# Optimization experiments

Hardware: AMD Instinct MI355X
Metric: run time of the kernel (lower is better)

Reference implementation:

```python
import jax, jax.numpy as jnp
import numpy as np

D = 1024
H = 16
HD = D // H
FF = 4096
EPS = 1e-5
B, L = 8, 1024

def setup_inputs() -> dict:
    key = jax.random.key(0)
    ks = jax.random.split(key, 12)
    s = lambda k, shape: jax.random.normal(k, shape, dtype=jnp.float32) * (shape[0] ** -0.5)
    return {
        "x": jax.random.normal(ks[0], (B, L, D), dtype=jnp.float32),
        "attention_mask": jnp.ones((B, L), dtype=jnp.int32),
        "wq": s(ks[1], (D, D)), "bq": jnp.zeros((D,), jnp.float32),
        "wk": s(ks[2], (D, D)), "bk": jnp.zeros((D,), jnp.float32),
        "wv": s(ks[3], (D, D)), "bv": jnp.zeros((D,), jnp.float32),
        "wo": s(ks[4], (D, D)), "bo": jnp.zeros((D,), jnp.float32),
        "ln1_s": jnp.ones((D,), jnp.float32), "ln1_b": jnp.zeros((D,), jnp.float32),
        "ln2_s": jnp.ones((D,), jnp.float32), "ln2_b": jnp.zeros((D,), jnp.float32),
        "w1": s(ks[5], (D, FF)), "b1": jnp.zeros((FF,), jnp.float32),
        "w2": s(ks[6], (FF, D)), "b2": jnp.zeros((D,), jnp.float32),
    }

def _layer_norm(x, scale, bias):
    mu = jnp.mean(x, axis=-1, keepdims=True)
    var = jnp.mean(jnp.square(x - mu), axis=-1, keepdims=True)
    return (x - mu) * jax.lax.rsqrt(var + EPS) * scale + bias

def _quick_gelu(x):
    return x * jax.nn.sigmoid(1.702 * x)

def reference(x, attention_mask, wq, bq, wk, bk, wv, bv, wo, bo,
              ln1_s, ln1_b, ln2_s, ln2_b, w1, b1, w2, b2):
    Bc, Lc, Dc = x.shape
    scale = HD ** -0.5
    # --- attention block (pre-LN) ---
    h = _layer_norm(x, ln1_s, ln1_b)
    to_heads = lambda t: t.reshape(Bc, Lc, H, HD).transpose(0, 2, 1, 3)
    q = to_heads(h @ wq + bq)
    k = to_heads(h @ wk + bk)
    v = to_heads(h @ wv + bv)
    scores = jnp.einsum('bhqd,bhkd->bhqk', q.astype(jnp.float32), k.astype(jnp.float32)) * scale
    fmask = jnp.where(attention_mask[:, None, None, :] > 0, 0.0,
                      jnp.finfo(scores.dtype).min)
    weights = jax.nn.softmax(scores + fmask, axis=-1)
    attn = jnp.einsum('bhqk,bhkd->bhqd', weights, v.astype(jnp.float32))
    attn = attn.transpose(0, 2, 1, 3).reshape(Bc, Lc, Dc).astype(x.dtype)
    x = x + (attn @ wo + bo)
    # --- MLP block (pre-LN) ---
    h = _layer_norm(x, ln2_s, ln2_b)
    h = _quick_gelu(h @ w1 + b1) @ w2 + b2
    return x + h
```

## Files before the change

### kernel.cpp

```cpp
#include <hip/hip_runtime.h>
#include <math.h>

#define D_MODEL 1024
#define N_TOK   8192
#define SEQ_L   1024
#define N_HEAD  16
#define HEAD_D  64
#define FF_DIM  4096

typedef __attribute__((ext_vector_type(8))) short bf16x8;
typedef __attribute__((ext_vector_type(4))) short short4v;
typedef __attribute__((ext_vector_type(2))) int  int2v;
typedef __attribute__((ext_vector_type(4))) float f32x4;

#define MFMA16(a, b, c) __builtin_amdgcn_mfma_f32_16x16x32_bf16((a), (b), (c), 0, 0, 0)

#define GLD16(gp, lp) __builtin_amdgcn_global_load_lds(                      \
    (const __attribute__((address_space(1))) void*)(gp),                     \
    (__attribute__((address_space(3))) void*)(lp), 16, 0, 0)

#if defined(__has_builtin)
#if __has_builtin(__builtin_amdgcn_exp2f)
#define EXP2F(x) __builtin_amdgcn_exp2f(x)
#else
#define EXP2F(x) exp2f(x)
#endif
#else
#define EXP2F(x) exp2f(x)
#endif

__device__ __forceinline__ short f2bf(float f) {
    unsigned u = __float_as_uint(f);
    u += 0x7fffu + ((u >> 16) & 1u);
    return (short)(u >> 16);
}

__device__ __forceinline__ int pack2bf(float a, float b) {
    unsigned ua = __float_as_uint(a) + 0x8000u;
    unsigned ub = __float_as_uint(b) + 0x8000u;
    return __builtin_amdgcn_perm(ub, ua, 0x07060302u);
}

__device__ __forceinline__ unsigned ldsoff(const void* p) {
    return (unsigned)(size_t)(const __attribute__((address_space(3))) void*)p;
}

__device__ __forceinline__ bf16x8 dsr(unsigned off) {
    bf16x8 d;
    asm volatile("ds_read_b128 %0, %1" : "=v"(d) : "v"(off));
    return d;
}

__global__ __launch_bounds__(256) void ln_kernel(const float* __restrict__ x,
                                                 const float* __restrict__ g,
                                                 const float* __restrict__ b,
                                                 short* __restrict__ o)
{
    int t = blockIdx.x;
    const float* xr = x + (size_t)t * D_MODEL;
    short* orow = o + (size_t)t * D_MODEL;
    float vals[4];
    float lsum = 0.f, lsq = 0.f;
#pragma unroll
    for (int i = 0; i < 4; i++) {
        float v = xr[threadIdx.x + i * 256];
        vals[i] = v; lsum += v; lsq += v * v;
    }
#pragma unroll
    for (int off = 32; off > 0; off >>= 1) {
        lsum += __shfl_down(lsum, off);
        lsq  += __shfl_down(lsq,  off);
    }
    __shared__ float red[8];
    int wid = threadIdx.x >> 6, lane = threadIdx.x & 63;
    if (lane == 0) { red[wid] = lsum; red[4 + wid] = lsq; }
    __syncthreads();
    if (threadIdx.x == 0) {
        red[0] = red[0] + red[1] + red[2] + red[3];
        red[4] = red[4] + red[5] + red[6] + red[7];
    }
    __syncthreads();
    float mean = red[0] * (1.f / D_MODEL);
    float var  = red[4] * (1.f / D_MODEL) - mean * mean;
    float inv  = rsqrtf(var + 1e-5f);
#pragma unroll
    for (int i = 0; i < 4; i++) {
        int c = threadIdx.x + i * 256;
        orow[c] = f2bf((vals[i] - mean) * inv * g[c] + b[c]);
    }
}

__global__ __launch_bounds__(256) void prep_kernel(
    const float* __restrict__ wq, const float* __restrict__ wk,
    const float* __restrict__ wv, const float* __restrict__ wo,
    const float* __restrict__ w1, const float* __restrict__ w2,
    const int*   __restrict__ amask,
    short* __restrict__ wqkvt, short* __restrict__ wot,
    short* __restrict__ w1t,  short* __restrict__ w2t,
    float* __restrict__ fmask)
{
    int id = blockIdx.x;
    if (id >= 12288) {
        int i = (id - 12288) * 256 + threadIdx.x;
        fmask[i] = (amask[i] > 0) ? 0.f : -1e30f;
        return;
    }
    const float* src; short* dst; int R, C, tloc, csh;
    if (id < 4096) {
        int wsel = id >> 10; tloc = id & 1023; R = 1024; C = 1024; csh = 5;
        src = (wsel == 0) ? wq : (wsel == 1) ? wk : (wsel == 2) ? wv : wo;
        dst = (wsel == 3) ? wot : (wqkvt + (size_t)wsel * 1024 * 1024);
    } else if (id < 8192) {
        tloc = id - 4096; R = 1024; C = 4096; csh = 7; src = w1; dst = w1t;
    } else {
        tloc = id - 8192; R = 4096; C = 1024; csh = 5; src = w2; dst = w2t;
    }
    int ty = tloc >> csh, tx = tloc & ((1 << csh) - 1);
    int r0 = ty * 32, c0 = tx * 32;
    __shared__ float t[32][33];
    int tid = threadIdx.x;
#pragma unroll
    for (int i = 0; i < 4; i++) {
        int idx = i * 256 + tid;
        int r = idx >> 5, c = idx & 31;
        t[r][c] = src[(size_t)(r0 + r) * C + c0 + c];
    }
    __syncthreads();
#pragma unroll
    for (int i = 0; i < 4; i++) {
        int idx = i * 256 + tid;
        int rr = idx >> 5, cc = idx & 31;
        dst[(size_t)(c0 + rr) * R + r0 + cc] = f2bf(t[cc][rr]);
    }
}

template<int DBUF>
__global__ __launch_bounds__(256) void gemm_bf16(
    const short* __restrict__ A, int lda,
    const short* __restrict__ Bt, int ldb,
    const float* __restrict__ bias,
    const float* __restrict__ bias2,
    const float* __restrict__ bias3,
    const float* __restrict__ resid,
    float* __restrict__ Cf, short* __restrict__ Cb, short* __restrict__ Cvt,
    int ldc, int K, int act, int qkv, int gx)
{
    __shared__ __align__(16) short sA[(1 + DBUF) * 8192];
    __shared__ __align__(16) short sB[(1 + DBUF) * 8192];
    const int tid = threadIdx.x;
    const int lane = tid & 63, wave = tid >> 6;
    const int quad = lane >> 4, l15 = lane & 15;

    const int id = blockIdx.x;
    const int xcd = id & 7, j = id >> 3;
    const int bx = j % gx, by = xcd + 8 * (j / gx);
    const int bm = by * 128, bn = bx * 128;
    const int wm = (wave >> 1) * 64, wn = (wave & 1) * 64;

    const int lr = lane >> 3;
    const int lc = (lane & 7) ^ lr;
    const int sw = l15 & 7;

    const short* Ab = A  + (size_t)(bm + wave * 32 + lr) * lda + lc * 8;
    const short* Bb = Bt + (size_t)(bn + wave * 32 + lr) * ldb + lc * 8;

    f32x4 acc[4][4];
#pragma unroll
    for (int i = 0; i < 4; i++)
#pragma unroll
        for (int jj = 0; jj < 4; jj++) acc[i][jj] = (f32x4){0.f, 0.f, 0.f, 0.f};

    const int nk = K >> 6;

    if (DBUF) {
#pragma unroll
        for (int c = 0; c < 4; c++) {
            int cid = wave * 4 + c;
            GLD16(Ab + (size_t)(c * 8) * lda, &sA[cid * 512]);
            GLD16(Bb + (size_t)(c * 8) * ldb, &sB[cid * 512]);
        }
    }

    for (int ki = 0; ki < nk; ki++) {
        __syncthreads();
        if (DBUF) {
            if (ki + 1 < nk) {
                int k0 = (ki + 1) << 6, nb = (ki + 1) & 1;
#pragma unroll
                for (int c = 0; c < 4; c++) {
                    int cid = wave * 4 + c;
                    GLD16(Ab + (size_t)(c * 8) * lda + k0, &sA[nb * 8192 + cid * 512]);
                    GLD16(Bb + (size_t)(c * 8) * ldb + k0, &sB[nb * 8192 + cid * 512]);
                }
            }
        } else {
            int k0 = ki << 6;
#pragma unroll
            for (int c = 0; c < 4; c++) {
                int cid = wave * 4 + c;
                GLD16(Ab + (size_t)(c * 8) * lda + k0, &sA[cid * 512]);
                GLD16(Bb + (size_t)(c * 8) * ldb + k0, &sB[cid * 512]);
            }
            __syncthreads();
        }
        const short* cA = &sA[DBUF ? (ki & 1) * 8192 : 0];
        const short* cB = &sB[DBUF ? (ki & 1) * 8192 : 0];
#pragma unroll
        for (int ko = 0; ko < 2; ko++) {
            bf16x8 af[4], bfr[4];
#pragma unroll
            for (int mt = 0; mt < 4; mt++) {
                int row = wm + mt * 16 + l15;
                af[mt] = *(const bf16x8*)&cA[(row * 8 + ((ko * 4 + quad) ^ sw)) * 8];
            }
#pragma unroll
            for (int nt = 0; nt < 4; nt++) {
                int row = wn + nt * 16 + l15;
                bfr[nt] = *(const bf16x8*)&cB[(row * 8 + ((ko * 4 + quad) ^ sw)) * 8];
            }
#pragma unroll
            for (int mt = 0; mt < 4; mt++)
#pragma unroll
                for (int nt = 0; nt < 4; nt++)
                    acc[mt][nt] = MFMA16(af[mt], bfr[nt], acc[mt][nt]);
        }
    }

#pragma unroll
    for (int mt = 0; mt < 4; mt++)
#pragma unroll
        for (int nt = 0; nt < 4; nt++) {
            int row0 = bm + wm + mt * 16 + quad * 4;
            int col  = bn + wn + nt * 16 + l15;
            if (qkv) {
                int seg = col >> 10, cloc = col & 1023;
                const float* bp = (seg == 0) ? bias : (seg == 1) ? bias2 : bias3;
                float bval = bp[cloc];
                if (seg == 2) {
                    int bb = row0 >> 10, l0 = row0 & 1023;
                    size_t page = (size_t)(bb * N_HEAD + (cloc >> 6)) * HEAD_D + (cloc & 63);
                    short4v pk = { f2bf(acc[mt][nt][0] + bval), f2bf(acc[mt][nt][1] + bval),
                                   f2bf(acc[mt][nt][2] + bval), f2bf(acc[mt][nt][3] + bval) };
                    *(short4v*)&Cvt[page * SEQ_L + l0] = pk;
                } else {
                    short* dst = Cb + (size_t)seg * ((size_t)N_TOK * D_MODEL);
#pragma unroll
                    for (int r = 0; r < 4; r++)
                        dst[(size_t)(row0 + r) * D_MODEL + cloc] = f2bf(acc[mt][nt][r] + bval);
                }
            } else {
#pragma unroll
                for (int r = 0; r < 4; r++) {
                    int row = row0 + r;
                    float v = acc[mt][nt][r] + bias[col];
                    if (act) v = v / (1.f + __expf(-1.702f * v));
                    if (resid) v += resid[(size_t)row * ldc + col];
                    if (Cb) Cb[(size_t)row * ldc + col] = f2bf(v);
                    else    Cf[(size_t)row * ldc + col] = v;
                }
            }
        }
}

#define BAR() __builtin_amdgcn_s_barrier()
#define WAIT_LGKM0() do { asm volatile("s_waitcnt lgkmcnt(0)");               \
                          __builtin_amdgcn_sched_barrier(0); } while (0)

#define STA(buf, h, tt) do {                                                  \
    const short* s_ = Asrc + (size_t)((h) * 128) * lda + (size_t)(tt) * 64;   \
    GLD16(s_,                    &sAs[(buf)*16384 + (h)*8192        + wave*512]); \
    GLD16(s_ + (size_t)64 * lda, &sAs[(buf)*16384 + (h)*8192 + 4096 + wave*512]); \
} while (0)

#define STB(buf, h, tt) do {                                                  \
    if constexpr (NREP == 4) {                                                \
        const short* s_ = Bsrc + (size_t)((h) * 128) * ldb + (size_t)(tt) * 64; \
        GLD16(s_,                    &sBs[(buf)*16384 + (h)*8192        + wave*512]); \
        GLD16(s_ + (size_t)64 * ldb, &sBs[(buf)*16384 + (h)*8192 + 4096 + wave*512]); \
    } else {                                                                  \
        const short* s_ = Bsrc + (size_t)((h) * 64) * ldb + (size_t)(tt) * 64; \
        GLD16(s_, &sBs[(buf)*8192 + (h)*4096 + wave*512]);                    \
    }                                                                         \
} while (0)

#define VMCNT() do {                                                          \
    if constexpr (NREP == 4) asm volatile("s_waitcnt vmcnt(6)");              \
    else                     asm volatile("s_waitcnt vmcnt(4)");              \
} while (0)

#define RDB(buf, nt) do {                                                     \
    unsigned r_ = bBase + (buf) * BUFB + ((unsigned)(wn + (nt)*16 + l15) << 7); \
    bfr[nt][0] = dsr(r_ + c0); bfr[nt][1] = dsr(r_ + c1);                     \
} while (0)
#define RDA(buf, mt8) do {                                                    \
    unsigned r_ = aBase + (buf) * 32768u + ((unsigned)(wm + (mt8)*16 + l15) << 7); \
    afr[(mt8) & 3][0] = dsr(r_ + c0); afr[(mt8) & 3][1] = dsr(r_ + c1);       \
} while (0)

#define PH_MFMA(mh, nh)                                                       \
    __builtin_amdgcn_s_setprio(1);                                            \
    _Pragma("unroll")                                                         \
    for (int mt = 0; mt < 4; mt++)                                            \
        _Pragma("unroll")                                                     \
        for (int nt = 0; nt < NREP / 2; nt++) {                               \
            acc[(mh)*4 + mt][(nh)*(NREP/2) + nt] =                            \
                MFMA16(afr[mt][0], bfr[(nh)*(NREP/2) + nt][0],                \
                       acc[(mh)*4 + mt][(nh)*(NREP/2) + nt]);                 \
            acc[(mh)*4 + mt][(nh)*(NREP/2) + nt] =                            \
                MFMA16(afr[mt][1], bfr[(nh)*(NREP/2) + nt][1],                \
                       acc[(mh)*4 + mt][(nh)*(NREP/2) + nt]);                 \
        }                                                                     \
    __builtin_amdgcn_s_setprio(0);

template<int NREP>
__global__ __launch_bounds__(512, 2) void gemm256(
    const short* __restrict__ A, int lda,
    const short* __restrict__ Bt, int ldb,
    const float* __restrict__ bias,
    const float* __restrict__ bias2,
    const float* __restrict__ bias3,
    const float* __restrict__ resid,
    float* __restrict__ Cf, short* __restrict__ Cb, short* __restrict__ Cvt,
    int ldc, int K, int act, int qkv, int gx)
{
    constexpr int BN = NREP * 64;
    constexpr unsigned BUFB = (unsigned)BN * 64u * 2u;
    __shared__ __align__(16) short sAs[2 * 256 * 64];
    __shared__ __align__(16) short sBs[2 * BN  * 64];

    const int tid  = threadIdx.x;
    const int wave = tid >> 6, lane = tid & 63;
    const int quad = lane >> 4, l15 = lane & 15;
    const int wm = (wave >> 2) * 128;
    const int wn = (wave & 3) * (NREP * 16);
    const int sw = l15 & 7;

    const unsigned aBase = ldsoff(sAs);
    const unsigned bBase = ldsoff(sBs);
    const unsigned c0 = (unsigned)((quad ^ sw) << 4);
    const unsigned c1 = c0 ^ 64u;

    const int id = blockIdx.x;
    const int xcd = id & 7, j = id >> 3;
    const int bx = j % gx, by = xcd + 8 * (j / gx);
    const int bm = by * 256, bn = bx * BN;

    const int r_in = tid >> 3;
    const int csrc = (tid & 7) ^ (r_in & 7);
    const short* Asrc = A  + (size_t)(bm + r_in) * lda + csrc * 8;
    const short* Bsrc = Bt + (size_t)(bn + r_in) * ldb + csrc * 8;

    f32x4 acc[8][NREP];
#pragma unroll
    for (int i = 0; i < 8; i++)
#pragma unroll
        for (int jj = 0; jj < NREP; jj++) acc[i][jj] = (f32x4){0.f, 0.f, 0.f, 0.f};

    const int nk = K >> 6;

    STB(0, 0, 0); STB(0, 1, 0);
    STA(0, 0, 0); STA(0, 1, 0);
    STB(1, 0, 1); STB(1, 1, 1);
    STA(1, 0, 1);
    VMCNT();
    BAR();

    bf16x8 afr[4][2], bfr[NREP][2];

    for (int it = 0; it < nk; it += 2) {
        int t2 = it + 2; if (t2 >= nk) t2 -= nk;
        int t3 = it + 3; if (t3 >= nk) t3 -= nk;

        RDB(0, 0); RDB(0, 1);
        RDA(0, 0); RDA(0, 1); RDA(0, 2); RDA(0, 3);
        STA(1, 1, it + 1);
        BAR(); WAIT_LGKM0();
        PH_MFMA(0, 0);
        BAR();
        if constexpr (NREP == 4) { RDB(0, 2); RDB(0, 3); }
        STB(0, 0, t2);
        BAR();
        if constexpr (NREP == 4) WAIT_LGKM0();
        PH_MFMA(0, 1);
        BAR();
        RDA(0, 4); RDA(0, 5); RDA(0, 6); RDA(0, 7);
        STB(0, 1, t2);
        BAR(); WAIT_LGKM0();
        PH_MFMA(1, 1);
        BAR();
        STA(0, 0, t2);
        BAR();
        PH_MFMA(1, 0);
        VMCNT();
        BAR();
        RDB(1, 0); RDB(1, 1);
        RDA(1, 0); RDA(1, 1); RDA(1, 2); RDA(1, 3);
        STA(0, 1, t2);
        BAR(); WAIT_LGKM0();
        PH_MFMA(0, 0);
        BAR();
        if constexpr (NREP == 4) { RDB(1, 2); RDB(1, 3); }
        STB(1, 0, t3);
        BAR();
        if constexpr (NREP == 4) WAIT_LGKM0();
        PH_MFMA(0, 1);
        BAR();
        RDA(1, 4); RDA(1, 5); RDA(1, 6); RDA(1, 7);
        STB(1, 1, t3);
        BAR(); WAIT_LGKM0();
        PH_MFMA(1, 1);
        BAR();
        STA(1, 0, t3);
        BAR();
        PH_MFMA(1, 0);
        VMCNT();
        BAR();
    }

#pragma unroll
    for (int mt = 0; mt < 8; mt++)
#pragma unroll
        for (int nt = 0; nt < NREP; nt++) {
            int row0 = bm + wm + mt * 16 + quad * 4;
            int col  = bn + wn + nt * 16 + l15;
            if (qkv) {
                int seg = col >> 10, cloc = col & 1023;
                const float* bp = (seg == 0) ? bias : (seg == 1) ? bias2 : bias3;
                float bval = bp[cloc];
                if (seg == 2) {
                    int bb = row0 >> 10, l0 = row0 & 1023;
                    size_t page = (size_t)(bb * N_HEAD + (cloc >> 6)) * HEAD_D + (cloc & 63);
                    short4v pk = { f2bf(acc[mt][nt][0] + bval), f2bf(acc[mt][nt][1] + bval),
                                   f2bf(acc[mt][nt][2] + bval), f2bf(acc[mt][nt][3] + bval) };
                    *(short4v*)&Cvt[page * SEQ_L + l0] = pk;
                } else {
                    short* dst = Cb + (size_t)seg * ((size_t)N_TOK * D_MODEL);
#pragma unroll
                    for (int r = 0; r < 4; r++)
                        dst[(size_t)(row0 + r) * D_MODEL + cloc] = f2bf(acc[mt][nt][r] + bval);
                }
            } else {
#pragma unroll
                for (int r = 0; r < 4; r++) {
                    int row = row0 + r;
                    float v = acc[mt][nt][r] + bias[col];
                    if (act) v = v / (1.f + __expf(-1.702f * v));
                    if (resid) v += resid[(size_t)row * ldc + col];
                    if (Cb) Cb[(size_t)row * ldc + col] = f2bf(v);
                    else    Cf[(size_t)row * ldc + col] = v;
                }
            }
        }
}

__global__ __launch_bounds__(256) void attn_kernel(
    const short* __restrict__ Q, const short* __restrict__ Kb,
    const short* __restrict__ Vt, const float* __restrict__ fmask,
    short* __restrict__ O)
{
    __shared__ __align__(16) short sK[8192];
    __shared__ __align__(16) short sV[8192];
    __shared__ __align__(16) short sP[4][32 * 136];
    __shared__ __align__(16) float sAl[4][2][20];

    const int g = blockIdx.x;
    const int xcd = g & 7, slot = g >> 3;
    const int qt = slot & 7, bhl = slot >> 3;
    const int bh = xcd * 16 + bhl;
    const int b = bh >> 4, h = bh & 15;

    const int tid = threadIdx.x;
    const int wave = tid >> 6, lane = tid & 63;
    const int quad = lane >> 4, l15 = lane & 15;

    const int qbase = b * SEQ_L + qt * 128;
    bf16x8 qf[2][2];
#pragma unroll
    for (int qh = 0; qh < 2; qh++) {
        const short* qp = Q + (size_t)(qbase + wave * 32 + qh * 16 + l15) * D_MODEL
                        + h * HEAD_D + quad * 8;
        qf[qh][0] = *(const bf16x8*)qp;
        qf[qh][1] = *(const bf16x8*)(qp + 32);
    }

    const short* Kbh = Kb + (size_t)b * SEQ_L * D_MODEL + h * HEAD_D;
    const short* Vbh = Vt + (size_t)(b * N_HEAD + h) * HEAD_D * SEQ_L;
    const float* mk  = fmask + b * SEQ_L;

    f32x4 o4[2][4];
#pragma unroll
    for (int qh = 0; qh < 2; qh++)
#pragma unroll
        for (int nt = 0; nt < 4; nt++) o4[qh][nt] = (f32x4){0.f, 0.f, 0.f, 0.f};
    float mrow[2] = {-1e30f, -1e30f}, lrow[2] = {0.f, 0.f};
    short* pslab = &sP[wave][0];
    const float CSC = 0.125f * 1.4426950408889634f;

    for (int kt = 0; kt < SEQ_L / 128; kt++) {
        __syncthreads();
#pragma unroll
        for (int j = 0; j < 4; j++) {
            int cid = wave * 4 + j;
            int kc = cid >> 1, key0 = (cid & 1) << 6;
            GLD16(Kbh + (size_t)(kt * 128 + key0 + lane) * D_MODEL + kc * 8,
                  &sK[cid * 512]);
            GLD16(Vbh + (size_t)lane * SEQ_L + kt * 128 + cid * 8,
                  &sV[cid * 512]);
        }
        __syncthreads();

        f32x4 mkv[8];
#pragma unroll
        for (int sub = 0; sub < 8; sub++)
            mkv[sub] = *(const f32x4*)&mk[kt * 128 + sub * 16 + quad * 4];

        f32x4 s[8][2];
#pragma unroll
        for (int sub = 0; sub < 8; sub++) {
            bf16x8 kf0 = *(const bf16x8*)&sK[(quad * 128 + sub * 16 + l15) * 8];
            bf16x8 kf1 = *(const bf16x8*)&sK[((quad + 4) * 128 + sub * 16 + l15) * 8];
#pragma unroll
            for (int qh = 0; qh < 2; qh++) {
                s[sub][qh] = (f32x4){0.f, 0.f, 0.f, 0.f};
                s[sub][qh] = MFMA16(kf0, qf[qh][0], s[sub][qh]);
                s[sub][qh] = MFMA16(kf1, qf[qh][1], s[sub][qh]);
            }
        }
        float alpha[2];
#pragma unroll
        for (int qh = 0; qh < 2; qh++) {
#pragma unroll
            for (int sub = 0; sub < 8; sub++)
#pragma unroll
                for (int r = 0; r < 4; r++)
                    s[sub][qh][r] = s[sub][qh][r] * CSC + mkv[sub][r];
            f32x4 mx4 = s[0][qh];
#pragma unroll
            for (int sub = 1; sub < 8; sub++)
#pragma unroll
                for (int r = 0; r < 4; r++) mx4[r] = fmaxf(mx4[r], s[sub][qh][r]);
            float pmax = fmaxf(fmaxf(mx4[0], mx4[1]), fmaxf(mx4[2], mx4[3]));
            pmax = fmaxf(pmax, __shfl_xor(pmax, 16));
            pmax = fmaxf(pmax, __shfl_xor(pmax, 32));
            float mnew = fmaxf(mrow[qh], pmax);
            alpha[qh] = EXP2F(mrow[qh] - mnew);
            mrow[qh] = mnew;
            if (quad == 0) sAl[wave][qh][l15] = alpha[qh];

            float ls = 0.f;
#pragma unroll
            for (int sub = 0; sub < 8; sub++) {
                float p0 = EXP2F(s[sub][qh][0] - mnew);
                float p1 = EXP2F(s[sub][qh][1] - mnew);
                float p2 = EXP2F(s[sub][qh][2] - mnew);
                float p3 = EXP2F(s[sub][qh][3] - mnew);
                ls += (p0 + p1) + (p2 + p3);
                int2v pk = { pack2bf(p0, p1), pack2bf(p2, p3) };
                *(int2v*)&pslab[(qh * 16 + l15) * 136 + sub * 16 + quad * 4] = pk;
            }
            ls += __shfl_xor(ls, 16);
            ls += __shfl_xor(ls, 32);
            lrow[qh] = lrow[qh] * alpha[qh] + ls;
        }

#pragma unroll
        for (int qh = 0; qh < 2; qh++) {
            f32x4 av = *(const f32x4*)&sAl[wave][qh][quad * 4];
#pragma unroll
            for (int nt = 0; nt < 4; nt++)
#pragma unroll
                for (int r = 0; r < 4; r++) o4[qh][nt][r] *= av[r];
        }

        bf16x8 pf[2][4];
#pragma unroll
        for (int qh = 0; qh < 2; qh++)
#pragma unroll
            for (int c = 0; c < 4; c++)
                pf[qh][c] = *(const bf16x8*)&pslab[(qh * 16 + l15) * 136 + c * 32 + quad * 8];
#pragma unroll
        for (int nt = 0; nt < 4; nt++)
#pragma unroll
            for (int c = 0; c < 4; c++) {
                bf16x8 vfr = *(const bf16x8*)&sV[((c * 4 + quad) * 64 + nt * 16 + l15) * 8];
                o4[0][nt] = MFMA16(pf[0][c], vfr, o4[0][nt]);
                o4[1][nt] = MFMA16(pf[1][c], vfr, o4[1][nt]);
            }
    }
    if (quad == 0) {
        sAl[wave][0][l15] = 1.f / lrow[0];
        sAl[wave][1][l15] = 1.f / lrow[1];
    }
    __syncthreads();
#pragma unroll
    for (int qh = 0; qh < 2; qh++) {
        f32x4 iv = *(const f32x4*)&sAl[wave][qh][quad * 4];
#pragma unroll
        for (int nt = 0; nt < 4; nt++)
#pragma unroll
            for (int r = 0; r < 4; r++)
                O[(size_t)(qbase + wave * 32 + qh * 16 + quad * 4 + r) * D_MODEL
                  + h * HEAD_D + nt * 16 + l15] = f2bf(o4[qh][nt][r] * iv[r]);
    }
}

extern "C" void kernel_launch(void* const* d_in, const int* in_sizes, int n_in,
                              void* d_out, int out_size, void* d_ws, size_t ws_size,
                              hipStream_t stream)
{
    const float* x     = (const float*)d_in[0];
    const int*   amask = (const int*)  d_in[1];
    const float* wq    = (const float*)d_in[2];
    const float* bq    = (const float*)d_in[3];
    const float* wk    = (const float*)d_in[4];
    const float* bk    = (const float*)d_in[5];
    const float* wv    = (const float*)d_in[6];
    const float* bv    = (const float*)d_in[7];
    const float* wo    = (const float*)d_in[8];
    const float* bo    = (const float*)d_in[9];
    const float* ln1s  = (const float*)d_in[10];
    const float* ln1b  = (const float*)d_in[11];
    const float* ln2s  = (const float*)d_in[12];
    const float* ln2b  = (const float*)d_in[13];
    const float* w1    = (const float*)d_in[14];
    const float* b1    = (const float*)d_in[15];
    const float* w2    = (const float*)d_in[16];
    const float* b2    = (const float*)d_in[17];
    float* out = (float*)d_out;

    char* w = (char*)d_ws;
    short* wqkvt = (short*)(w + (size_t)0);
    short* wot   = (short*)(w + ((size_t)6  << 20));
    short* w1t   = (short*)(w + ((size_t)8  << 20));
    short* w2t   = (short*)(w + ((size_t)16 << 20));
    short* hb    = (short*)(w + ((size_t)24 << 20));
    short* qb    = (short*)(w + ((size_t)40 << 20));
    short* kbf   = (short*)(w + ((size_t)56 << 20));
    short* attnb = (short*)(w + ((size_t)72 << 20));
    short* vtb   = (short*)(w + ((size_t)88 << 20));
    short* ffb   = qb;
    float* fmaskb = (float*)d_out;

    dim3 blk(256), blk512(512);

    prep_kernel<<<dim3(12320), blk, 0, stream>>>(wq, wk, wv, wo, w1, w2, amask,
                                                 wqkvt, wot, w1t, w2t, fmaskb);

    ln_kernel<<<N_TOK, blk, 0, stream>>>(x, ln1s, ln1b, hb);

    gemm_bf16<0><<<dim3(24 * 64), blk, 0, stream>>>(
        hb, 1024, wqkvt, 1024, bq, bk, bv, nullptr,
        nullptr, qb, vtb, 1024, 1024, 0, 1, 24);

    attn_kernel<<<dim3(1024), blk, 0, stream>>>(qb, kbf, vtb, fmaskb, attnb);

    gemm_bf16<1><<<dim3(8 * 64), blk, 0, stream>>>(
        attnb, 1024, wot, 1024, bo, nullptr, nullptr, x,
        out, nullptr, nullptr, 1024, 1024, 0, 0, 8);

    ln_kernel<<<N_TOK, blk, 0, stream>>>(out, ln2s, ln2b, hb);

    gemm256<4><<<dim3(512), blk512, 0, stream>>>(
        hb, 1024, w1t, 1024, b1, nullptr, nullptr, nullptr,
        nullptr, ffb, nullptr, 4096, 1024, 1, 0, 16);
    gemm256<2><<<dim3(256), blk512, 0, stream>>>(
        ffb, 4096, w2t, 4096, b2, nullptr, nullptr, out,
        out, nullptr, nullptr, 1024, 4096, 0, 0, 8);
}
```

Before: 612.3 us.

## Double-buffer fragment registers and interleave wave tiles in GEMM pipeline

The GEMM main loop is reordered so that A/B fragment registers are double-buffered per LDS stage, and the global-to-LDS prefetch schedule is changed: fewer barriers, different placement of STA/STB and the vmcnt waits. The mapping of waves to output tiles also changes from contiguous blocks to interleaved 16-row/16-column strips, which alters LDS read patterns. The aim is to overlap LDS reads with MFMA work and cut barrier stalls. In exchange it uses more VGPRs, which could hurt occupancy at 2 blocks/CU, and a wrong vmcnt or prefetch ordering could introduce races.

Measured after the change: 590.7 us. -3.5%, faster.

```diff
diff --git a/kernel.cpp b/kernel.cpp
--- a/kernel.cpp
+++ b/kernel.cpp
@@ -284,30 +284,34 @@
 } while (0)
 
 #define VMCNT() do {                                                          \
-    if constexpr (NREP == 4) asm volatile("s_waitcnt vmcnt(6)");              \
-    else                     asm volatile("s_waitcnt vmcnt(4)");              \
+    if constexpr (NREP == 4) asm volatile("s_waitcnt vmcnt(4)");              \
+    else                     asm volatile("s_waitcnt vmcnt(2)");              \
 } while (0)
 
 #define RDB(buf, nt) do {                                                     \
-    unsigned r_ = bBase + (buf) * BUFB + ((unsigned)(wn + (nt)*16 + l15) << 7); \
-    bfr[nt][0] = dsr(r_ + c0); bfr[nt][1] = dsr(r_ + c1);                     \
+    unsigned r_ = bBase + (buf) * BBUF                                        \
+                + ((unsigned)((nt) * 64 + wni + l15) << 7);                   \
+    bfr[buf][nt][0] = dsr(r_ + c0); bfr[buf][nt][1] = dsr(r_ + c1);           \
 } while (0)
 #define RDA(buf, mt8) do {                                                    \
-    unsigned r_ = aBase + (buf) * 32768u + ((unsigned)(wm + (mt8)*16 + l15) << 7); \
-    afr[(mt8) & 3][0] = dsr(r_ + c0); afr[(mt8) & 3][1] = dsr(r_ + c1);       \
+    unsigned r_ = aBase + (buf) * 32768u                                      \
+                + ((unsigned)((((mt8) >> 2) * 128) + (((mt8) & 3) * 32)       \
+                              + wmi + l15) << 7);                             \
+    afr[buf][(mt8) & 3][0] = dsr(r_ + c0);                                    \
+    afr[buf][(mt8) & 3][1] = dsr(r_ + c1);                                    \
 } while (0)
 
-#define PH_MFMA(mh, nh)                                                       \
+#define PH_MFMA(set, mh, nh)                                                  \
     __builtin_amdgcn_s_setprio(1);                                            \
     _Pragma("unroll")                                                         \
     for (int mt = 0; mt < 4; mt++)                                            \
         _Pragma("unroll")                                                     \
         for (int nt = 0; nt < NREP / 2; nt++) {                               \
             acc[(mh)*4 + mt][(nh)*(NREP/2) + nt] =                            \
-                MFMA16(afr[mt][0], bfr[(nh)*(NREP/2) + nt][0],                \
+                MFMA16(afr[set][mt][0], bfr[set][(nh)*(NREP/2) + nt][0],      \
                        acc[(mh)*4 + mt][(nh)*(NREP/2) + nt]);                 \
             acc[(mh)*4 + mt][(nh)*(NREP/2) + nt] =                            \
-                MFMA16(afr[mt][1], bfr[(nh)*(NREP/2) + nt][1],                \
+                MFMA16(afr[set][mt][1], bfr[set][(nh)*(NREP/2) + nt][1],      \
                        acc[(mh)*4 + mt][(nh)*(NREP/2) + nt]);                 \
         }                                                                     \
     __builtin_amdgcn_s_setprio(0);
@@ -324,15 +328,15 @@
     int ldc, int K, int act, int qkv, int gx)
 {
     constexpr int BN = NREP * 64;
-    constexpr unsigned BUFB = (unsigned)BN * 64u * 2u;
+    constexpr unsigned BBUF = (unsigned)BN * 64u * 2u;
     __shared__ __align__(16) short sAs[2 * 256 * 64];
     __shared__ __align__(16) short sBs[2 * BN  * 64];
 
     const int tid  = threadIdx.x;
     const int wave = tid >> 6, lane = tid & 63;
     const int quad = lane >> 4, l15 = lane & 15;
-    const int wm = (wave >> 2) * 128;
-    const int wn = (wave & 3) * (NREP * 16);
+    const int wmi = (wave >> 2) * 16;
+    const int wni = (wave & 3) * 16;
     const int sw = l15 & 7;
 
     const unsigned aBase = ldsoff(sAs);
@@ -361,68 +365,62 @@
     STB(0, 0, 0); STB(0, 1, 0);
     STA(0, 0, 0); STA(0, 1, 0);
     STB(1, 0, 1); STB(1, 1, 1);
-    STA(1, 0, 1);
     VMCNT();
     BAR();
 
-    bf16x8 afr[4][2], bfr[NREP][2];
+    bf16x8 afr[2][4][2], bfr[2][NREP][2];
 
     for (int it = 0; it < nk; it += 2) {
+        const int t1 = it + 1;
         int t2 = it + 2; if (t2 >= nk) t2 -= nk;
         int t3 = it + 3; if (t3 >= nk) t3 -= nk;
 
-        RDB(0, 0); RDB(0, 1);
+        RDB(0, 0);
+        if constexpr (NREP == 4) RDB(0, 1);
         RDA(0, 0); RDA(0, 1); RDA(0, 2); RDA(0, 3);
-        STA(1, 1, it + 1);
+        STA(1, 0, t1);
         BAR(); WAIT_LGKM0();
-        PH_MFMA(0, 0);
-        BAR();
+        PH_MFMA(0, 0, 0);
         if constexpr (NREP == 4) { RDB(0, 2); RDB(0, 3); }
+        else                     { RDB(0, 1); }
+        STA(1, 1, t1);
+        BAR(); WAIT_LGKM0();
+        PH_MFMA(0, 0, 1);
+        RDA(0, 4); RDA(0, 5); RDA(0, 6); RDA(0, 7);
         STB(0, 0, t2);
-        BAR();
-        if constexpr (NREP == 4) WAIT_LGKM0();
-        PH_MFMA(0, 1);
-        BAR();
-        RDA(0, 4); RDA(0, 5); RDA(0, 6); RDA(0, 7);
+        BAR(); WAIT_LGKM0();
+        PH_MFMA(0, 1, 1);
         STB(0, 1, t2);
-        BAR(); WAIT_LGKM0();
-        PH_MFMA(1, 1);
-        BAR();
-        STA(0, 0, t2);
-        BAR();
-        PH_MFMA(1, 0);
         VMCNT();
         BAR();
-        RDB(1, 0); RDB(1, 1);
+        PH_MFMA(0, 1, 0);
+        RDB(1, 0);
+        if constexpr (NREP == 4) RDB(1, 1);
         RDA(1, 0); RDA(1, 1); RDA(1, 2); RDA(1, 3);
+        STA(0, 0, t2);
+        BAR(); WAIT_LGKM0();
+        PH_MFMA(1, 0, 0);
+        if constexpr (NREP == 4) { RDB(1, 2); RDB(1, 3); }
+        else                     { RDB(1, 1); }
         STA(0, 1, t2);
         BAR(); WAIT_LGKM0();
-        PH_MFMA(0, 0);
-        BAR();
-        if constexpr (NREP == 4) { RDB(1, 2); RDB(1, 3); }
+        PH_MFMA(1, 0, 1);
+        RDA(1, 4); RDA(1, 5); RDA(1, 6); RDA(1, 7);
         STB(1, 0, t3);
-        BAR();
-        if constexpr (NREP == 4) WAIT_LGKM0();
-        PH_MFMA(0, 1);
-        BAR();
-        RDA(1, 4); RDA(1, 5); RDA(1, 6); RDA(1, 7);
+        BAR(); WAIT_LGKM0();
+        PH_MFMA(1, 1, 1);
         STB(1, 1, t3);
-        BAR(); WAIT_LGKM0();
-        PH_MFMA(1, 1);
-        BAR();
-        STA(1, 0, t3);
-        BAR();
-        PH_MFMA(1, 0);
         VMCNT();
         BAR();
+        PH_MFMA(1, 1, 0);
     }
 
 #pragma unroll
     for (int mt = 0; mt < 8; mt++)
 #pragma unroll
         for (int nt = 0; nt < NREP; nt++) {
-            int row0 = bm + wm + mt * 16 + quad * 4;
-            int col  = bn + wn + nt * 16 + l15;
+            int row0 = bm + (mt >> 2) * 128 + (mt & 3) * 32 + wmi + quad * 4;
+            int col  = bn + nt * 64 + wni + l15;
             if (qkv) {
                 int seg = col >> 10, cloc = col & 1023;
                 const float* bp = (seg == 0) ? bias : (seg == 1) ? bias2 : bias3;
```
